# Optimization experiments

Hardware: AMD Instinct MI355X
Metric: run time of the kernel (lower is better)

The kernel has to match this reference:

```python
import jax, jax.numpy as jnp
import numpy as np

WS = 11      # window_size
C = 3        # channels
SIGMA = 1.5
C1 = 0.01 ** 2
C2 = 0.03 ** 2


def _gaussian_window():
    # 1D gaussian, normalized, then outer product -> [C, 1, WS, WS] depthwise kernel
    x = jnp.arange(WS, dtype=jnp.float32)
    g = jnp.exp(-((x - WS // 2) ** 2) / (2.0 * SIGMA ** 2))
    g = g / g.sum()
    w2d = jnp.outer(g, g)  # [WS, WS]
    return jnp.broadcast_to(w2d[None, None], (C, 1, WS, WS))


def _dwconv(x, w):
    # depthwise conv2d, SAME padding (pad = WS//2, odd kernel)
    pad = WS // 2
    return jax.lax.conv_general_dilated(
        x, w, window_strides=(1, 1), padding=[(pad, pad), (pad, pad)],
        dimension_numbers=("NCHW", "OIHW", "NCHW"), feature_group_count=C)


def setup_inputs() -> dict:
    key = jax.random.key(0)
    k1, k2 = jax.random.split(key)
    pred = jax.random.uniform(k1, (16, 3, 512, 512), dtype=jnp.float32)
    target = jax.random.uniform(k2, (16, 3, 512, 512), dtype=jnp.float32)
    return {"pred": pred, "target": target}


def reference(pred, target):
    w = _gaussian_window()
    mu1 = _dwconv(pred, w)
    mu2 = _dwconv(target, w)
    mu1_sq = mu1 * mu1
    mu2_sq = mu2 * mu2
    mu1_mu2 = mu1 * mu2
    sigma1_sq = _dwconv(pred * pred, w) - mu1_sq
    sigma2_sq = _dwconv(target * target, w) - mu2_sq
    sigma12 = _dwconv(pred * target, w) - mu1_mu2
    ssim_map = ((2.0 * mu1_mu2 + C1) * (2.0 * sigma12 + C2)) / (
        (mu1_sq + mu2_sq + C1) * (sigma1_sq + sigma2_sq + C2))
    return 1.0 - ssim_map.mean()
```

## Files before the change

### kernel.cpp

```cpp
#include <hip/hip_runtime.h>


#define IMG 512
#define NCHAN 48
#define TW 32
#define TH 64
#define HR (TH + 10)
#define PST 33

typedef float v2f __attribute__((ext_vector_type(2)));
typedef float v4f __attribute__((ext_vector_type(4)));

constexpr double RW1 = 0.8007374029168082;
constexpr double RW2 = 0.4111122905071876;
constexpr double RW3 = 0.1353352832366127;
constexpr double RW4 = 0.0285655007845504;
constexpr double RW5 = 0.0038659201394728;
constexpr double RSUM = 1.0 + 2.0 * (RW1 + RW2 + RW3 + RW4 + RW5);
constexpr float GW[11] = {
    (float)(RW5 / RSUM), (float)(RW4 / RSUM), (float)(RW3 / RSUM),
    (float)(RW2 / RSUM), (float)(RW1 / RSUM), (float)(1.0 / RSUM),
    (float)(RW1 / RSUM), (float)(RW2 / RSUM), (float)(RW3 / RSUM),
    (float)(RW4 / RSUM), (float)(RW5 / RSUM)};

__device__ __forceinline__ v2f pk_fma(v2f a, v2f b, v2f c) {
  v2f d;
  asm("v_pk_fma_f32 %0, %1, %2, %3" : "=v"(d) : "v"(a), "v"(b), "v"(c));
  return d;
}
__device__ __forceinline__ v2f pk_mul(v2f a, v2f b) {
  v2f d;
  asm("v_pk_mul_f32 %0, %1, %2" : "=v"(d) : "v"(a), "v"(b));
  return d;
}

template <bool CHECKED>
__device__ __forceinline__ void hload(const float* __restrict__ P,
                                      const float* __restrict__ T, int r0t,
                                      int c0, int j, v4f* vp, v4f* vt) {
  const int g = j & 7;
  const int h = j >> 3;
  const int gy = r0t - 5 + h;
  const int gx0 = c0 + g * 4 - 8;
  if (CHECKED) {
    const bool rowok = (gy >= 0) && (gy < IMG);
    const float* __restrict__ Prow = P + (size_t)gy * IMG;
    const float* __restrict__ Trow = T + (size_t)gy * IMG;
#pragma unroll
    for (int q = 0; q < 5; ++q) {
      const int gx = gx0 + q * 4;
      vp[q] = (v4f){0.f, 0.f, 0.f, 0.f};
      vt[q] = vp[q];
      if (rowok && gx >= 0 && gx < IMG) {
        vp[q] = *(const v4f*)(Prow + gx);
        vt[q] = *(const v4f*)(Trow + gx);
      }
    }
  } else {
    const float* __restrict__ Prow = P + (size_t)gy * IMG + gx0;
    const float* __restrict__ Trow = T + (size_t)gy * IMG + gx0;
#pragma unroll
    for (int q = 0; q < 5; ++q) {
      vp[q] = *(const v4f*)(Prow + q * 4);
      vt[q] = *(const v4f*)(Trow + q * 4);
    }
  }
}

__device__ __forceinline__ void hcompute(int j, const v4f* vp, const v4f* vt,
                                         float4 (*hs)[PST]) {
  const int g = j & 7;
  const int h = j >> 3;
  v2f uv[20], sq[20];
#pragma unroll
  for (int q = 0; q < 5; ++q) {
    const v4f p4 = vp[q], t4 = vt[q];
    uv[q * 4 + 0] = (v2f){p4.x + t4.x, p4.x - t4.x};
    uv[q * 4 + 1] = (v2f){p4.y + t4.y, p4.y - t4.y};
    uv[q * 4 + 2] = (v2f){p4.z + t4.z, p4.z - t4.z};
    uv[q * 4 + 3] = (v2f){p4.w + t4.w, p4.w - t4.w};
  }
#pragma unroll
  for (int i = 3; i <= 16; ++i) sq[i] = pk_mul(uv[i], uv[i]);
#pragma unroll
  for (int o = 0; o < 4; ++o) {
    v2f amu = (v2f){0.f, 0.f};
    v2f asq = (v2f){0.f, 0.f};
#pragma unroll
    for (int k = 0; k < 11; ++k) {
      const v2f w = (v2f){GW[k], GW[k]};
      amu = pk_fma(uv[3 + o + k], w, amu);
      asq = pk_fma(sq[3 + o + k], w, asq);
    }
    hs[h][g * 4 + o] = make_float4(amu.x, amu.y, asq.x, asq.y);
  }
}

template <bool CHECKED>
__device__ __forceinline__ void phase_b(const float* __restrict__ P,
                                        const float* __restrict__ T, int r0t,
                                        int c0, int tid, float4 (*hs)[PST]) {
  v4f ap[5], at[5], bp[5], bt[5], cp[5], ct[5];
  const bool hasC = tid < (HR * 8 - 512);
  hload<CHECKED>(P, T, r0t, c0, tid, ap, at);
  hload<CHECKED>(P, T, r0t, c0, tid + 256, bp, bt);
  if (hasC) hload<CHECKED>(P, T, r0t, c0, tid + 512, cp, ct);
  __builtin_amdgcn_sched_barrier(0);
  hcompute(tid, ap, at, hs);
  hcompute(tid + 256, bp, bt, hs);
  if (hasC) hcompute(tid + 512, cp, ct, hs);
}

__global__ __launch_bounds__(256, 2) void ssim_main(
    const float* __restrict__ pred, const float* __restrict__ tgt,
    double* __restrict__ ws) {
  __shared__ float4 hs[HR][PST];
  __shared__ float wsum[4];

  const int tid = threadIdx.x;
  const int c0 = blockIdx.x * TW;
  const int r0t = blockIdx.y * TH;
  const int nc = blockIdx.z;
  const size_t base = (size_t)nc * IMG * IMG;
  const float* __restrict__ P = pred + base;
  const float* __restrict__ T = tgt + base;

  const bool interior =
      (c0 != 0) && (c0 != IMG - TW) && (r0t != 0) && (r0t != IMG - TH);
  if (interior)
    phase_b<false>(P, T, r0t, c0, tid, hs);
  else
    phase_b<true>(P, T, r0t, c0, tid, hs);
  __syncthreads();

  float lsum = 0.f;
  {
    const int x = tid & (TW - 1);
    const int r0 = (tid >> 5) * 8;
    v2f amu[8], asq[8];
#pragma unroll
    for (int o = 0; o < 8; ++o) {
      amu[o] = (v2f){0.f, 0.f};
      asq[o] = (v2f){0.f, 0.f};
    }
#pragma unroll
    for (int j = 0; j < 18; ++j) {
      const float4 h4 = hs[r0 + j][x];
      const v2f hmu = (v2f){h4.x, h4.y};
      const v2f hsq = (v2f){h4.z, h4.w};
#pragma unroll
      for (int o = 0; o < 8; ++o) {
        const int k = j - o;
        if (k >= 0 && k < 11) {
          const v2f w = (v2f){GW[k], GW[k]};
          amu[o] = pk_fma(hmu, w, amu[o]);
          asq[o] = pk_fma(hsq, w, asq[o]);
        }
      }
    }
#pragma unroll
    for (int o = 0; o < 8; ++o) {
      const v2f m2 = pk_mul(amu[o], amu[o]);
      const float cusq = m2.x, cvsq = m2.y;
      const float cu2 = asq[o].x, cv2 = asq[o].y;
      const float mu12 = 0.25f * (cusq - cvsq);
      const float musq = 0.5f * (cusq + cvsq);
      const float s12 = 0.25f * (cu2 - cv2);
      const float ssq = 0.5f * (cu2 + cv2);
      const float num = (2.f * mu12 + 1e-4f) * (2.f * (s12 - mu12) + 9e-4f);
      const float den = (musq + 1e-4f) * (ssq - musq + 9e-4f);
      lsum += num * __builtin_amdgcn_rcpf(den);
    }
  }

#pragma unroll
  for (int off = 32; off > 0; off >>= 1) lsum += __shfl_down(lsum, off, 64);
  if ((tid & 63) == 0) wsum[tid >> 6] = lsum;
  __syncthreads();
  if (tid == 0) {
    const float bsum = wsum[0] + wsum[1] + wsum[2] + wsum[3];
    unsafeAtomicAdd(&ws[nc], (double)bsum);
  }
}

__global__ void ssim_fin(const double* __restrict__ ws,
                         float* __restrict__ out) {
  const int l = threadIdx.x;
  double v = (l < NCHAN) ? ws[l] : 0.0;
#pragma unroll
  for (int off = 32; off > 0; off >>= 1) v += __shfl_down(v, off, 64);
  if (l == 0) out[0] = (float)(1.0 - v / (double)(IMG * IMG * NCHAN));
}

extern "C" void kernel_launch(void* const* d_in, const int* in_sizes, int n_in,
                              void* d_out, int out_size, void* d_ws,
                              size_t ws_size, hipStream_t stream) {
  const float* pred = (const float*)d_in[0];
  const float* tgt = (const float*)d_in[1];
  double* ws = (double*)d_ws;

  hipMemsetAsync(d_ws, 0, NCHAN * sizeof(double), stream);
  dim3 grid(IMG / TW, IMG / TH, NCHAN);
  ssim_main<<<grid, 256, 0, stream>>>(pred, tgt, ws);
  ssim_fin<<<1, 64, 0, stream>>>(ws, (float*)d_out);
}
```

Baseline: 171.5 us.

## Raise occupancy to 4 blocks/CU, serialize third load, fuse final reduction

Launch bounds go from 2 to 4 blocks per CU, and the third horizontal-load batch now reuses the first set of registers after they are consumed, which lowers register pressure. The separate finalize kernel is replaced by a last-block-done pattern that uses an atomic counter, so the final reduction happens inside the main kernel and one launch is saved. The cost is less memory-level parallelism, since the third load is no longer issued together with the others, plus one extra atomic per block. Dropping the sched_barrier lets the compiler interleave loads and compute as it chooses.

```diff
diff --git a/kernel.cpp b/kernel.cpp
--- a/kernel.cpp
+++ b/kernel.cpp
@@ -7,6 +7,7 @@
 #define TH 64
 #define HR (TH + 10)
 #define PST 33
+#define NBLK ((IMG / TW) * (IMG / TH) * NCHAN)
 
 typedef float v2f __attribute__((ext_vector_type(2)));
 typedef float v4f __attribute__((ext_vector_type(4)));
@@ -100,20 +101,20 @@
 __device__ __forceinline__ void phase_b(const float* __restrict__ P,
                                         const float* __restrict__ T, int r0t,
                                         int c0, int tid, float4 (*hs)[PST]) {
-  v4f ap[5], at[5], bp[5], bt[5], cp[5], ct[5];
-  const bool hasC = tid < (HR * 8 - 512);
+  v4f ap[5], at[5], bp[5], bt[5];
   hload<CHECKED>(P, T, r0t, c0, tid, ap, at);
   hload<CHECKED>(P, T, r0t, c0, tid + 256, bp, bt);
-  if (hasC) hload<CHECKED>(P, T, r0t, c0, tid + 512, cp, ct);
-  __builtin_amdgcn_sched_barrier(0);
   hcompute(tid, ap, at, hs);
   hcompute(tid + 256, bp, bt, hs);
-  if (hasC) hcompute(tid + 512, cp, ct, hs);
-}
-
-__global__ __launch_bounds__(256, 2) void ssim_main(
+  if (tid < HR * 8 - 512) {
+    hload<CHECKED>(P, T, r0t, c0, tid + 512, ap, at);
+    hcompute(tid + 512, ap, at, hs);
+  }
+}
+
+__global__ __launch_bounds__(256, 4) void ssim_main(
     const float* __restrict__ pred, const float* __restrict__ tgt,
-    double* __restrict__ ws) {
+    double* __restrict__ ws, float* __restrict__ out) {
   __shared__ float4 hs[HR][PST];
   __shared__ float wsum[4];
 
@@ -180,16 +181,18 @@
   if (tid == 0) {
     const float bsum = wsum[0] + wsum[1] + wsum[2] + wsum[3];
     unsafeAtomicAdd(&ws[nc], (double)bsum);
-  }
-}
-
-__global__ void ssim_fin(const double* __restrict__ ws,
-                         float* __restrict__ out) {
-  const int l = threadIdx.x;
-  double v = (l < NCHAN) ? ws[l] : 0.0;
-#pragma unroll
-  for (int off = 32; off > 0; off >>= 1) v += __shfl_down(v, off, 64);
-  if (l == 0) out[0] = (float)(1.0 - v / (double)(IMG * IMG * NCHAN));
+    __threadfence();
+    unsigned* cnt = (unsigned*)(ws + NCHAN);
+    const unsigned old = __hip_atomic_fetch_add(cnt, 1u, __ATOMIC_ACQ_REL,
+                                                __HIP_MEMORY_SCOPE_AGENT);
+    if (old == NBLK - 1) {
+      double s = 0.0;
+      for (int i = 0; i < NCHAN; ++i)
+        s += __hip_atomic_load(&ws[i], __ATOMIC_RELAXED,
+                               __HIP_MEMORY_SCOPE_AGENT);
+      out[0] = (float)(1.0 - s / (double)((size_t)IMG * IMG * NCHAN));
+    }
+  }
 }
 
 extern "C" void kernel_launch(void* const* d_in, const int* in_sizes, int n_in,
@@ -199,8 +202,7 @@
   const float* tgt = (const float*)d_in[1];
   double* ws = (double*)d_ws;
 
-  hipMemsetAsync(d_ws, 0, NCHAN * sizeof(double), stream);
+  hipMemsetAsync(d_ws, 0, NCHAN * sizeof(double) + sizeof(unsigned), stream);
   dim3 grid(IMG / TW, IMG / TH, NCHAN);
-  ssim_main<<<grid, 256, 0, stream>>>(pred, tgt, ws);
-  ssim_fin<<<1, 64, 0, stream>>>(ws, (float*)d_out);
-}
+  ssim_main<<<grid, 256, 0, stream>>>(pred, tgt, ws, (float*)d_out);
+}
```

Measured after the change: 576.9 us. 236% more time.

## Stage interior tile rows into LDS via global_load_lds, compute horizontal pass in place

Applied to the files above, without the earlier changes.

For interior tiles, each row of raw pred and target data (the tile plus halo) is now copied straight into shared memory with the async global-to-LDS load. The horizontal Gaussian pass then reads overlapping windows from shared memory and writes its results back into the same row buffer, instead of each thread issuing five overlapping 16-byte global loads. Launch bounds are raised to four blocks per CU to allow more occupancy. This cuts redundant global and L1 traffic, but adds a block barrier before compute and relies on each row's reads and in-place writes staying inside one wavefront.

```diff
diff --git a/kernel.cpp b/kernel.cpp
--- a/kernel.cpp
+++ b/kernel.cpp
@@ -6,7 +6,7 @@
 #define TW 32
 #define TH 64
 #define HR (TH + 10)
-#define PST 33
+#define RST 33
 
 typedef float v2f __attribute__((ext_vector_type(2)));
 typedef float v4f __attribute__((ext_vector_type(4)));
@@ -34,43 +34,14 @@
   return d;
 }
 
-template <bool CHECKED>
-__device__ __forceinline__ void hload(const float* __restrict__ P,
-                                      const float* __restrict__ T, int r0t,
-                                      int c0, int j, v4f* vp, v4f* vt) {
-  const int g = j & 7;
-  const int h = j >> 3;
-  const int gy = r0t - 5 + h;
-  const int gx0 = c0 + g * 4 - 8;
-  if (CHECKED) {
-    const bool rowok = (gy >= 0) && (gy < IMG);
-    const float* __restrict__ Prow = P + (size_t)gy * IMG;
-    const float* __restrict__ Trow = T + (size_t)gy * IMG;
-#pragma unroll
-    for (int q = 0; q < 5; ++q) {
-      const int gx = gx0 + q * 4;
-      vp[q] = (v4f){0.f, 0.f, 0.f, 0.f};
-      vt[q] = vp[q];
-      if (rowok && gx >= 0 && gx < IMG) {
-        vp[q] = *(const v4f*)(Prow + gx);
-        vt[q] = *(const v4f*)(Trow + gx);
-      }
-    }
-  } else {
-    const float* __restrict__ Prow = P + (size_t)gy * IMG + gx0;
-    const float* __restrict__ Trow = T + (size_t)gy * IMG + gx0;
-#pragma unroll
-    for (int q = 0; q < 5; ++q) {
-      vp[q] = *(const v4f*)(Prow + q * 4);
-      vt[q] = *(const v4f*)(Trow + q * 4);
-    }
-  }
-}
-
-__device__ __forceinline__ void hcompute(int j, const v4f* vp, const v4f* vt,
-                                         float4 (*hs)[PST]) {
-  const int g = j & 7;
-  const int h = j >> 3;
+__device__ __forceinline__ void gload_lds16(const float* g, float4* l) {
+  __builtin_amdgcn_global_load_lds(
+      (const __attribute__((address_space(1))) void*)g,
+      (__attribute__((address_space(3))) void*)l, 16, 0, 0);
+}
+
+__device__ __forceinline__ void hcompute_w(const v4f* vp, const v4f* vt,
+                                           float4* dst) {
   v2f uv[20], sq[20];
 #pragma unroll
   for (int q = 0; q < 5; ++q) {
@@ -92,29 +63,51 @@
       amu = pk_fma(uv[3 + o + k], w, amu);
       asq = pk_fma(sq[3 + o + k], w, asq);
     }
-    hs[h][g * 4 + o] = make_float4(amu.x, amu.y, asq.x, asq.y);
-  }
-}
-
-template <bool CHECKED>
-__device__ __forceinline__ void phase_b(const float* __restrict__ P,
-                                        const float* __restrict__ T, int r0t,
-                                        int c0, int tid, float4 (*hs)[PST]) {
-  v4f ap[5], at[5], bp[5], bt[5], cp[5], ct[5];
-  const bool hasC = tid < (HR * 8 - 512);
-  hload<CHECKED>(P, T, r0t, c0, tid, ap, at);
-  hload<CHECKED>(P, T, r0t, c0, tid + 256, bp, bt);
-  if (hasC) hload<CHECKED>(P, T, r0t, c0, tid + 512, cp, ct);
-  __builtin_amdgcn_sched_barrier(0);
-  hcompute(tid, ap, at, hs);
-  hcompute(tid + 256, bp, bt, hs);
-  if (hasC) hcompute(tid + 512, cp, ct, hs);
-}
-
-__global__ __launch_bounds__(256, 2) void ssim_main(
+    dst[o] = make_float4(amu.x, amu.y, asq.x, asq.y);
+  }
+}
+
+__device__ __forceinline__ void item_fast(int j, float4* lds4) {
+  const int g = j & 7;
+  const int h = j >> 3;
+  float4* row = lds4 + h * RST;
+  v4f p4[5], t4[5];
+#pragma unroll
+  for (int q = 0; q < 5; ++q) {
+    p4[q] = *(const v4f*)(row + g + q);
+    t4[q] = *(const v4f*)(row + 12 + g + q);
+  }
+  hcompute_w(p4, t4, row + 4 * g);
+}
+
+__device__ __forceinline__ void item_chk(const float* __restrict__ P,
+                                         const float* __restrict__ T, int r0t,
+                                         int c0, int j, float4* lds4) {
+  const int g = j & 7;
+  const int h = j >> 3;
+  const int gy = r0t - 5 + h;
+  const int gx0 = c0 + g * 4 - 8;
+  const bool rowok = (gy >= 0) && (gy < IMG);
+  const float* __restrict__ Prow = P + (size_t)gy * IMG;
+  const float* __restrict__ Trow = T + (size_t)gy * IMG;
+  v4f p4[5], t4[5];
+#pragma unroll
+  for (int q = 0; q < 5; ++q) {
+    const int gx = gx0 + q * 4;
+    p4[q] = (v4f){0.f, 0.f, 0.f, 0.f};
+    t4[q] = p4[q];
+    if (rowok && gx >= 0 && gx < IMG) {
+      p4[q] = *(const v4f*)(Prow + gx);
+      t4[q] = *(const v4f*)(Trow + gx);
+    }
+  }
+  hcompute_w(p4, t4, lds4 + h * RST + 4 * g);
+}
+
+__global__ __launch_bounds__(256, 4) void ssim_main(
     const float* __restrict__ pred, const float* __restrict__ tgt,
     double* __restrict__ ws) {
-  __shared__ float4 hs[HR][PST];
+  __shared__ float4 lds4[HR * RST];
   __shared__ float wsum[4];
 
   const int tid = threadIdx.x;
@@ -127,10 +120,25 @@
 
   const bool interior =
       (c0 != 0) && (c0 != IMG - TW) && (r0t != 0) && (r0t != IMG - TH);
-  if (interior)
-    phase_b<false>(P, T, r0t, c0, tid, hs);
-  else
-    phase_b<true>(P, T, r0t, c0, tid, hs);
+
+  if (interior) {
+    const int lane = tid & 63;
+    const int wv = tid >> 6;
+    const int q = (lane < 12) ? lane : lane - 12;
+    const float* arr = (lane < 12) ? P : T;
+    const float* srcbase = arr + (size_t)(r0t - 5) * IMG + (c0 - 8) + q * 4;
+    for (int r = wv; r < HR; r += 4) {
+      if (lane < 24) gload_lds16(srcbase + (size_t)r * IMG, lds4 + r * RST);
+    }
+    __syncthreads();
+    item_fast(tid, lds4);
+    item_fast(tid + 256, lds4);
+    if (tid < HR * 8 - 512) item_fast(tid + 512, lds4);
+  } else {
+    item_chk(P, T, r0t, c0, tid, lds4);
+    item_chk(P, T, r0t, c0, tid + 256, lds4);
+    if (tid < HR * 8 - 512) item_chk(P, T, r0t, c0, tid + 512, lds4);
+  }
   __syncthreads();
 
   float lsum = 0.f;
@@ -145,7 +153,7 @@
     }
 #pragma unroll
     for (int j = 0; j < 18; ++j) {
-      const float4 h4 = hs[r0 + j][x];
+      const float4 h4 = lds4[(r0 + j) * RST + x];
       const v2f hmu = (v2f){h4.x, h4.y};
       const v2f hsq = (v2f){h4.z, h4.w};
 #pragma unroll
```

After: 166.9 us. 1.03x faster.
